# Kernel tuning notes

Hardware: AMD Instinct MI355X
Metric: run time of the kernel (lower is better)

## Reference

```python
import jax, jax.numpy as jnp
import numpy as np

B, SQ, C = 8, 4096, 1280
CAD = 2048
H, D = 20, 64          # heads x head_dim = hidden_size
NT = 4                 # num IP tokens
TXT = 77               # text tokens
IP_SCALE = 1.0


def setup_inputs() -> dict:
    key = jax.random.key(0)
    ks = jax.random.split(key, 9)
    s = 0.02
    return {
        "hidden_states": jax.random.normal(ks[0], (B, SQ, C), jnp.float32),
        "encoder_hidden_states": jax.random.normal(ks[1], (B, TXT + NT, CAD), jnp.float32),
        "Wq": jax.random.normal(ks[2], (C, C), jnp.float32) * s,
        "Wk": jax.random.normal(ks[3], (CAD, C), jnp.float32) * s,
        "Wv": jax.random.normal(ks[4], (CAD, C), jnp.float32) * s,
        "Wk_ip": jax.random.normal(ks[5], (CAD, C), jnp.float32) * s,
        "Wv_ip": jax.random.normal(ks[6], (CAD, C), jnp.float32) * s,
        "Wo": jax.random.normal(ks[7], (C, C), jnp.float32) * s,
        "bo": jnp.zeros((C,), jnp.float32),
    }


def _heads(x):
    # [b, s, C] -> [b, H, s, D]
    b, s, _ = x.shape
    return x.reshape(b, s, H, D).transpose(0, 2, 1, 3)


def _attend(q, k, v):
    scale = jnp.asarray(1.0 / np.sqrt(D), q.dtype)
    probs = jax.nn.softmax(jnp.einsum('bhqd,bhkd->bhqk', q, k) * scale, axis=-1)
    return jnp.einsum('bhqk,bhkd->bhqd', probs, v)


def reference(hidden_states, encoder_hidden_states, Wq, Wk, Wv, Wk_ip, Wv_ip, Wo, bo):
    residual = hidden_states
    txt = encoder_hidden_states[:, :-NT, :]   # [B, 77, CAD]
    ip = encoder_hidden_states[:, -NT:, :]    # [B, 4, CAD]

    q = _heads(hidden_states @ Wq)            # [B, H, SQ, D]
    k = _heads(txt @ Wk)
    v = _heads(txt @ Wv)
    out = _attend(q, k, v)                    # text branch

    ip_k = _heads(ip @ Wk_ip)
    ip_v = _heads(ip @ Wv_ip)
    out = out + IP_SCALE * _attend(q, ip_k, ip_v)  # IP-adapter branch

    b = out.shape[0]
    out = out.transpose(0, 2, 1, 3).reshape(b, SQ, C)  # merge heads
    out = out @ Wo + bo
    return out + residual
```

## Files before the change

kernel.cpp:

```cpp
#include <hip/hip_runtime.h>
#include <hip/hip_bf16.h>
#include <cstdint>
#include <cstddef>


typedef __bf16 bf16_t;
typedef __bf16 bf16x8 __attribute__((ext_vector_type(8)));
typedef __bf16 bf16x4 __attribute__((ext_vector_type(4)));
typedef float  f32x4  __attribute__((ext_vector_type(4)));
typedef unsigned int u32x4 __attribute__((ext_vector_type(4)));

using as3_void  = __attribute__((address_space(3))) void;
using as1_cvoid = const __attribute__((address_space(1))) void;

#define TXT_ 77

__device__ __forceinline__ bf16x8 ld16(const void* p) {
  u32x4 v = *(const u32x4*)p;
  return __builtin_bit_cast(bf16x8, v);
}

template <int EPI>
__global__ __launch_bounds__(512, 2)
void gemm256(const bf16_t* __restrict__ A, const bf16_t* __restrict__ Bt,
             void* __restrict__ Cout, int ntn, int N, int K,
             const float* __restrict__ bias, const void* __restrict__ residual)
{
  __shared__ __align__(16) char smem[131072];
  const int tid = threadIdx.x, lane = tid & 63, wid = tid >> 6;
  const int wm = wid >> 2, wn = wid & 3;

  const int nwg = gridDim.x;
  int g = blockIdx.x;
  if ((nwg & 7) == 0) g = (blockIdx.x & 7) * (nwg >> 3) + (blockIdx.x >> 3);
  const long bm = (long)(g / ntn) * 256;
  const long bn = (long)(g % ntn) * 256;
  const int NTk = K >> 5;

  const int srow = lane >> 2;
  const int scol = ((lane & 3) ^ ((lane >> 3) & 3)) * 8;

  auto stageA = [&](int t) {
    const int buf = t & 3;
    const long k0 = (long)t << 5;
#pragma unroll
    for (int j = 0; j < 2; ++j) {
      const int ci = j * 8 + wid;
      const bf16_t* gp = A + (bm + ci * 16 + srow) * (long)K + k0 + scol;
      __builtin_amdgcn_global_load_lds((as1_cvoid*)gp,
          (as3_void*)(smem + buf * 16384 + ci * 1024), 16, 0, 0);
    }
  };
  auto stageB = [&](int t) {
    const int buf = t & 3;
    const long k0 = (long)t << 5;
#pragma unroll
    for (int j = 0; j < 2; ++j) {
      const int ci = j * 8 + wid;
      const bf16_t* gp = Bt + (bn + ci * 16 + srow) * (long)K + k0 + scol;
      __builtin_amdgcn_global_load_lds((as1_cvoid*)gp,
          (as3_void*)(smem + 65536 + buf * 16384 + ci * 1024), 16, 0, 0);
    }
  };

  const int l15 = lane & 15, kq = lane >> 4;
  const int rc16 = (kq ^ ((l15 >> 1) & 3)) << 4;

  f32x4 acc[8][4] = {};
  bf16x8 afr[4], bfr[4];

  stageA(0); stageB(0); stageA(1); stageB(1);
  asm volatile("s_waitcnt vmcnt(4)" ::: "memory");
  __builtin_amdgcn_s_barrier();

  for (int t = 0; t < NTk; ++t) {
    const char* sa = smem + (t & 3) * 16384;
    const char* sb = smem + 65536 + (t & 3) * 16384;
    const bool pf = (t + 2 < NTk);

#pragma unroll
    for (int n = 0; n < 4; ++n)
      bfr[n] = ld16(sb + (wn * 64 + n * 16 + l15) * 64 + rc16);
#pragma unroll
    for (int m = 0; m < 4; ++m)
      afr[m] = ld16(sa + (wm * 128 + m * 16 + l15) * 64 + rc16);
    if (pf) stageA(t + 2);
    __builtin_amdgcn_s_setprio(1);
#pragma unroll
    for (int m = 0; m < 4; ++m)
#pragma unroll
      for (int n = 0; n < 4; ++n)
        acc[m][n] = __builtin_amdgcn_mfma_f32_16x16x32_bf16(afr[m], bfr[n], acc[m][n], 0, 0, 0);
    __builtin_amdgcn_s_setprio(0);

#pragma unroll
    for (int m = 0; m < 4; ++m)
      afr[m] = ld16(sa + (wm * 128 + (m + 4) * 16 + l15) * 64 + rc16);
    if (pf) stageB(t + 2);
    __builtin_amdgcn_s_setprio(1);
#pragma unroll
    for (int m = 0; m < 4; ++m)
#pragma unroll
      for (int n = 0; n < 4; ++n)
        acc[m + 4][n] = __builtin_amdgcn_mfma_f32_16x16x32_bf16(afr[m], bfr[n], acc[m + 4][n], 0, 0, 0);
    __builtin_amdgcn_s_setprio(0);

    if (t == NTk - 2) asm volatile("s_waitcnt vmcnt(0)" ::: "memory");
    else              asm volatile("s_waitcnt vmcnt(4)" ::: "memory");
    __builtin_amdgcn_s_barrier();
  }

  const int orow0 = (lane >> 4) << 2;
  if constexpr (EPI == 0) {
    bf16_t* cl = (bf16_t*)smem;
    const int lrow0 = wm * 128 + orow0;
    const int lcol0 = wn * 64 + l15;
#pragma unroll
    for (int m = 0; m < 8; ++m)
#pragma unroll
      for (int n = 0; n < 4; ++n)
#pragma unroll
        for (int r = 0; r < 4; ++r)
          cl[(lrow0 + m * 16 + r) * 256 + lcol0 + n * 16] = (bf16_t)acc[m][n][r];
    __syncthreads();
    const int rr = tid >> 5, cc = tid & 31;
#pragma unroll
    for (int s = 0; s < 16; ++s) {
      const int row = s * 16 + rr;
      const u32x4 v = *(const u32x4*)(cl + row * 256 + cc * 8);
      *(u32x4*)((bf16_t*)Cout + (bm + row) * (long)N + bn + cc * 8) = v;
    }
  } else {
#pragma unroll
    for (int m = 0; m < 8; ++m) {
#pragma unroll
      for (int n = 0; n < 4; ++n) {
        const long col = bn + wn * 64 + n * 16 + l15;
#pragma unroll
        for (int r = 0; r < 4; ++r) {
          const long row = bm + wm * 128 + m * 16 + orow0 + r;
          ((float*)Cout)[row * N + col] =
              acc[m][n][r] + bias[col] +
              (float)((const bf16_t*)residual)[row * N + col];
        }
      }
    }
  }
}

__global__ __launch_bounds__(256, 4)
void gemm_small(const bf16_t* __restrict__ A0, const bf16_t* __restrict__ B0,
                bf16_t* __restrict__ C0,
                const bf16_t* __restrict__ A1, const bf16_t* __restrict__ B1,
                bf16_t* __restrict__ C1)
{
  __shared__ __align__(16) char smem[2][16384];
  const int tid  = threadIdx.x;
  const int lane = tid & 63;
  const int wid  = tid >> 6;
  const int wm = wid >> 1, wn = wid & 1;

  const bf16_t *A, *Bt;
  bf16_t* Cout;
  int g = blockIdx.x;
  if (g < 100) { A = A0; Bt = B0; Cout = C0; }
  else         { A = A1; Bt = B1; Cout = C1; g -= 100; }
  const int ntn = 20, N = 2560, K = 2048;

  const long bm = (long)(g / ntn) * 128;
  const long bn = (long)(g % ntn) * 128;

  f32x4 acc[4][4] = {};

  const int srow = lane >> 2;
  const int skb  = (lane & 3) ^ (((lane >> 2) ^ (lane >> 4)) & 3);
  const int NT = K >> 5;

  auto stage = [&](int buf, int kt) {
    const int k0 = kt << 5;
#pragma unroll
    for (int cc = 0; cc < 2; ++cc) {
      const int c = wid + cc * 4;
      const bf16_t* ga = A + (bm + c * 16 + srow) * (long)K + (k0 + skb * 8);
      __builtin_amdgcn_global_load_lds((as1_cvoid*)ga,
                                       (as3_void*)(&smem[buf][c * 1024]), 16, 0, 0);
      const bf16_t* gb = Bt + (bn + c * 16 + srow) * (long)K + (k0 + skb * 8);
      __builtin_amdgcn_global_load_lds((as1_cvoid*)gb,
                                       (as3_void*)(&smem[buf][8192 + c * 1024]), 16, 0, 0);
    }
  };

  const int rkb    = (((lane >> 4) ^ (lane & 3) ^ ((lane >> 2) & 3)) & 3) << 4;
  const int rrow_a = wm * 64 + (lane & 15);
  const int rrow_b = wn * 64 + (lane & 15);

  stage(0, 0);
  int cur = 0;
  for (int t = 0; t < NT; ++t) {
    __syncthreads();
    if (t + 1 < NT) stage(cur ^ 1, t + 1);
    const char* sa = smem[cur];
    const char* sb = smem[cur] + 8192;
    bf16x8 af[4], bfv[4];
#pragma unroll
    for (int m = 0; m < 4; ++m)
      af[m] = ld16(sa + (rrow_a + m * 16) * 64 + rkb);
#pragma unroll
    for (int n = 0; n < 4; ++n)
      bfv[n] = ld16(sb + (rrow_b + n * 16) * 64 + rkb);
#pragma unroll
    for (int m = 0; m < 4; ++m)
#pragma unroll
      for (int n = 0; n < 4; ++n)
        acc[m][n] = __builtin_amdgcn_mfma_f32_16x16x32_bf16(af[m], bfv[n], acc[m][n], 0, 0, 0);
    cur ^= 1;
  }

  const int orow0 = wm * 64 + ((lane >> 4) << 2);
  const int ocol0 = wn * 64 + (lane & 15);
#pragma unroll
  for (int m = 0; m < 4; ++m)
#pragma unroll
    for (int n = 0; n < 4; ++n) {
      const long col = bn + ocol0 + n * 16;
#pragma unroll
      for (int r = 0; r < 4; ++r)
        Cout[(bm + orow0 + m * 16 + r) * (long)N + col] = (bf16_t)acc[m][n][r];
    }
}

__global__ __launch_bounds__(256, 3)
void attn_fused(const bf16_t* __restrict__ q, const bf16_t* __restrict__ kvt,
                const bf16_t* __restrict__ kvip, bf16_t* __restrict__ outp)
{
  __shared__ __align__(16) bf16_t K_lds[80 * 64];
  __shared__ __align__(16) bf16_t Kip_lds[16 * 64];
  __shared__ __align__(16) bf16_t Vt_lds[64 * 128];
  __shared__ __align__(16) bf16_t P_lds[4][16 * 128];

  const int tid = threadIdx.x, lane = tid & 63, wid = tid >> 6;
  const int h = blockIdx.y, b = blockIdx.z;
  const int kvcol = h << 6;

  for (int idx = tid; idx < 640; idx += 256) {
    const int j = idx >> 3, c = idx & 7;
    bf16x8 v = {};
    if (j < TXT_) v = ld16(kvt + (long)(b * 80 + j) * 2560 + kvcol + c * 8);
    *(bf16x8*)((char*)K_lds + j * 128 + ((c ^ (j & 7)) << 4)) = v;
  }
  if (tid < 128) {
    const int j = tid >> 3, c = tid & 7;
    bf16x8 v = {};
    if (j < 4) v = ld16(kvip + (long)(b * 4 + j) * 2560 + kvcol + c * 8);
    *(bf16x8*)((char*)Kip_lds + j * 128 + ((c ^ (j & 7)) << 4)) = v;
  }
  for (int idx = tid; idx < 1024; idx += 256) {
    const int key = idx >> 3, c = idx & 7;
    bf16x8 v = {};
    if (key < TXT_)
      v = ld16(kvt + (long)(b * 80 + key) * 2560 + 1280 + kvcol + c * 8);
    else if (key >= 96 && key < 100)
      v = ld16(kvip + (long)(b * 4 + key - 96) * 2560 + 1280 + kvcol + c * 8);
#pragma unroll
    for (int e = 0; e < 8; ++e) {
      const int d = c * 8 + e;
      *(bf16_t*)((char*)Vt_lds + d * 256 + ((key * 2) ^ ((d & 7) << 4))) = v[e];
    }
  }
  for (int idx = tid; idx < 1024; idx += 256)
    *(bf16x8*)((char*)P_lds + idx * 16) = (bf16x8){};
  __syncthreads();

  const int l15 = lane & 15, hi = lane >> 4;
  const int dblk = hi << 3;
  const int prow0 = hi << 2;
  const float scale = 0.125f;
  char* const pw = (char*)P_lds[wid];

  const long qrow0 = (long)b * 4096 + ((long)blockIdx.x << 8) + (wid << 6);
  bf16x8 qf[4][2];
#pragma unroll
  for (int ms = 0; ms < 4; ++ms) {
    const bf16_t* qp = q + (qrow0 + ms * 16 + l15) * 1280 + kvcol;
    qf[ms][0] = ld16(qp + dblk);
    qf[ms][1] = ld16(qp + 32 + dblk);
  }

#pragma unroll
  for (int ms = 0; ms < 4; ++ms) {
    f32x4 sc[5];
#pragma unroll
    for (int t = 0; t < 5; ++t) {
      const int j = (t << 4) + l15;
      const bf16x8 k0 = ld16((char*)K_lds + j * 128 + ((hi ^ (j & 7)) << 4));
      const bf16x8 k1 = ld16((char*)K_lds + j * 128 + (((4 + hi) ^ (j & 7)) << 4));
      f32x4 z = {0.f, 0.f, 0.f, 0.f};
      z = __builtin_amdgcn_mfma_f32_16x16x32_bf16(qf[ms][0], k0, z, 0, 0, 0);
      z = __builtin_amdgcn_mfma_f32_16x16x32_bf16(qf[ms][1], k1, z, 0, 0, 0);
      sc[t] = z;
    }
#pragma unroll
    for (int t = 0; t < 5; ++t) {
      const bool valid = ((t << 4) + l15) < TXT_;
#pragma unroll
      for (int r = 0; r < 4; ++r)
        sc[t][r] = valid ? sc[t][r] * scale : -1e30f;
    }

#pragma unroll
    for (int r = 0; r < 4; ++r) {
      float m = sc[0][r];
#pragma unroll
      for (int t = 1; t < 5; ++t) m = fmaxf(m, sc[t][r]);
      m = fmaxf(m, __shfl_xor(m, 1));
      m = fmaxf(m, __shfl_xor(m, 2));
      m = fmaxf(m, __shfl_xor(m, 4));
      m = fmaxf(m, __shfl_xor(m, 8));
      float l = 0.f;
#pragma unroll
      for (int t = 0; t < 5; ++t) { const float p = __expf(sc[t][r] - m); sc[t][r] = p; l += p; }
      l += __shfl_xor(l, 1);
      l += __shfl_xor(l, 2);
      l += __shfl_xor(l, 4);
      l += __shfl_xor(l, 8);
      const float inv = 1.f / l;
      const int row = prow0 + r;
#pragma unroll
      for (int t = 0; t < 5; ++t)
        *(bf16_t*)(pw + row * 256 + ((((t << 4) + l15) * 2) ^ ((row & 7) << 4))) =
            (bf16_t)(sc[t][r] * inv);
    }

    {
      const bf16x8 ki0 = ld16((char*)Kip_lds + l15 * 128 + ((hi ^ (l15 & 7)) << 4));
      const bf16x8 ki1 = ld16((char*)Kip_lds + l15 * 128 + (((4 + hi) ^ (l15 & 7)) << 4));
      f32x4 z = {0.f, 0.f, 0.f, 0.f};
      z = __builtin_amdgcn_mfma_f32_16x16x32_bf16(qf[ms][0], ki0, z, 0, 0, 0);
      z = __builtin_amdgcn_mfma_f32_16x16x32_bf16(qf[ms][1], ki1, z, 0, 0, 0);
      const bool vip = l15 < 4;
#pragma unroll
      for (int r = 0; r < 4; ++r) {
        const float s = vip ? z[r] * scale : -1e30f;
        float m = s;
        m = fmaxf(m, __shfl_xor(m, 1));
        m = fmaxf(m, __shfl_xor(m, 2));
        m = fmaxf(m, __shfl_xor(m, 4));
        m = fmaxf(m, __shfl_xor(m, 8));
        const float p = __expf(s - m);
        float l = p;
        l += __shfl_xor(l, 1);
        l += __shfl_xor(l, 2);
        l += __shfl_xor(l, 4);
        l += __shfl_xor(l, 8);
        const int row = prow0 + r;
        *(bf16_t*)(pw + row * 256 + (((96 + l15) * 2) ^ ((row & 7) << 4))) =
            (bf16_t)(p * (1.f / l));
      }
    }

    f32x4 o[4] = {};
#pragma unroll
    for (int s = 0; s < 4; ++s) {
      const bf16x8 pa =
          ld16(pw + l15 * 256 + ((((s << 2) + hi) << 4) ^ ((l15 & 7) << 4)));
#pragma unroll
      for (int n = 0; n < 4; ++n) {
        const int d = (n << 4) + l15;
        const bf16x8 vb =
            ld16((char*)Vt_lds + d * 256 + ((((s << 2) + hi) << 4) ^ ((d & 7) << 4)));
        o[n] = __builtin_amdgcn_mfma_f32_16x16x32_bf16(pa, vb, o[n], 0, 0, 0);
      }
    }

    const long orow = qrow0 + ms * 16 + prow0;
#pragma unroll
    for (int n = 0; n < 4; ++n)
#pragma unroll
      for (int r = 0; r < 4; ++r)
        outp[(orow + r) * 1280 + kvcol + (n << 4) + l15] = (bf16_t)o[n][r];
  }
}

__global__ void cvt_bf16(const float* __restrict__ in, bf16_t* __restrict__ out, long n)
{
  const long i = ((long)blockIdx.x * 256 + threadIdx.x) * 4;
  if (i >= n) return;
  const float4 v = *(const float4*)(in + i);
  bf16x4 r;
  r[0] = (bf16_t)v.x; r[1] = (bf16_t)v.y; r[2] = (bf16_t)v.z; r[3] = (bf16_t)v.w;
  *(bf16x4*)(out + i) = r;
}

__global__ void transpose_all(const float* __restrict__ Wq, const float* __restrict__ Wo,
                              const float* __restrict__ Wk, const float* __restrict__ Wv,
                              const float* __restrict__ Wki, const float* __restrict__ Wvi,
                              bf16_t* __restrict__ Wq_t, bf16_t* __restrict__ Wo_t,
                              bf16_t* __restrict__ Wkv_t, bf16_t* __restrict__ Wip_t)
{
  const int z = blockIdx.z;
  const float* in;
  bf16_t* out;
  int K;
  switch (z) {
    case 0:  in = Wq;  out = Wq_t;                        K = 1280; break;
    case 1:  in = Wo;  out = Wo_t;                        K = 1280; break;
    case 2:  in = Wk;  out = Wkv_t;                       K = 2048; break;
    case 3:  in = Wv;  out = Wkv_t + (long)1280 * 2048;   K = 2048; break;
    case 4:  in = Wki; out = Wip_t;                       K = 2048; break;
    default: in = Wvi; out = Wip_t + (long)1280 * 2048;   K = 2048; break;
  }
  const int k0 = blockIdx.x * 32, n0 = blockIdx.y * 32;
  if (k0 >= K) return;
  __shared__ float tile[32][33];
  for (int i = threadIdx.y; i < 32; i += 8)
    tile[i][threadIdx.x] = in[(long)(k0 + i) * 1280 + n0 + threadIdx.x];
  __syncthreads();
  for (int i = threadIdx.y; i < 32; i += 8)
    out[(long)(n0 + i) * K + k0 + threadIdx.x] = (bf16_t)tile[threadIdx.x][i];
}

__global__ void pack_enc(const float* __restrict__ enc, bf16_t* __restrict__ a_txt,
                         bf16_t* __restrict__ a_ip)
{
  const long t4 = ((long)blockIdx.x * 256 + threadIdx.x) * 4;
  const long NTXT = 640L * 2048;
  bf16x4 r;
  r[0] = r[1] = r[2] = r[3] = (bf16_t)0.f;
  if (t4 < NTXT) {
    const int row = (int)(t4 >> 11), col = (int)(t4 & 2047);
    const int b = row / 80, j = row - b * 80;
    if (j < TXT_) {
      const float4 v = *(const float4*)(enc + (((long)(b * 81 + j)) << 11) + col);
      r[0] = (bf16_t)v.x; r[1] = (bf16_t)v.y; r[2] = (bf16_t)v.z; r[3] = (bf16_t)v.w;
    }
    *(bf16x4*)(a_txt + t4) = r;
  } else {
    const long u = t4 - NTXT;
    const int row = (int)(u >> 11), col = (int)(u & 2047);
    if (row < 32) {
      const int b = row >> 2, j = row & 3;
      const float4 v = *(const float4*)(enc + (((long)(b * 81 + TXT_ + j)) << 11) + col);
      r[0] = (bf16_t)v.x; r[1] = (bf16_t)v.y; r[2] = (bf16_t)v.z; r[3] = (bf16_t)v.w;
    }
    *(bf16x4*)(a_ip + u) = r;
  }
}

extern "C" void kernel_launch(void* const* d_in, const int* in_sizes, int n_in,
                              void* d_out, int out_size, void* d_ws, size_t ws_size,
                              hipStream_t stream)
{
  (void)in_sizes; (void)n_in; (void)out_size; (void)ws_size;
  const float* hs  = (const float*)d_in[0];
  const float* enc = (const float*)d_in[1];
  const float* Wq  = (const float*)d_in[2];
  const float* Wk  = (const float*)d_in[3];
  const float* Wv  = (const float*)d_in[4];
  const float* Wki = (const float*)d_in[5];
  const float* Wvi = (const float*)d_in[6];
  const float* Wo  = (const float*)d_in[7];
  const float* bo  = (const float*)d_in[8];

  char* ws = (char*)d_ws;
  size_t off = 0;
  auto alloc = [&](size_t bytes) {
    char* p = ws + off;
    off += (bytes + 255) & ~(size_t)255;
    return p;
  };
  bf16_t* buf1   = (bf16_t*)alloc(83886080);
  bf16_t* qb     = (bf16_t*)alloc(83886080);
  bf16_t* Wq_t   = (bf16_t*)alloc(3276800);
  bf16_t* Wo_t   = (bf16_t*)alloc(3276800);
  bf16_t* Wkv_t  = (bf16_t*)alloc(10485760);
  bf16_t* Wip_t  = (bf16_t*)alloc(10485760);
  bf16_t* a_txt  = (bf16_t*)alloc(2621440);
  bf16_t* a_ip   = (bf16_t*)alloc(524288);
  bf16_t* kv_txt = (bf16_t*)alloc(3276800);
  bf16_t* kv_ip  = (bf16_t*)alloc(655360);

  cvt_bf16<<<40960, 256, 0, stream>>>(hs, buf1, 41943040L);
  transpose_all<<<dim3(64, 40, 6), dim3(32, 8), 0, stream>>>(
      Wq, Wo, Wk, Wv, Wki, Wvi, Wq_t, Wo_t, Wkv_t, Wip_t);
  pack_enc<<<1536, 256, 0, stream>>>(enc, a_txt, a_ip);

  gemm256<0><<<640, 512, 0, stream>>>(buf1, Wq_t, qb, 5, 1280, 1280,
                                      nullptr, nullptr);
  gemm_small<<<120, 256, 0, stream>>>(a_txt, Wkv_t, kv_txt, a_ip, Wip_t, kv_ip);

  attn_fused<<<dim3(16, 20, 8), 256, 0, stream>>>(qb, kv_txt, kv_ip, qb);

  gemm256<2><<<640, 512, 0, stream>>>(qb, Wo_t, d_out, 5, 1280, 1280,
                                      bo, buf1);
}
```

Measured before the change: 439.8 us.

## Fuse fp32-to-bf16 conversion of hidden states into Q-projection GEMM A-loading

Removes the standalone cvt_bf16 pass over hidden_states. The Q GEMM now loads fp32 A tiles into registers, converts them to bf16 and writes them to LDS itself, and the output GEMM reads the fp32 residual directly. This cuts a full read/write pass over the 168MB input and its bf16 copy. In exchange, the Q GEMM A path moves from direct global-to-LDS loads to register staging, with twice the global bytes per tile and extra VGPR pressure.

Result: slower. 470.7 us (+7.0%).

```diff
diff --git a/kernel.cpp b/kernel.cpp
--- a/kernel.cpp
+++ b/kernel.cpp
@@ -20,11 +20,11 @@
   return __builtin_bit_cast(bf16x8, v);
 }
 
-template <int EPI>
+template <int EPI, int AF32>
 __global__ __launch_bounds__(512, 2)
-void gemm256(const bf16_t* __restrict__ A, const bf16_t* __restrict__ Bt,
+void gemm256(const void* __restrict__ Ap, const bf16_t* __restrict__ Bt,
              void* __restrict__ Cout, int ntn, int N, int K,
-             const float* __restrict__ bias, const void* __restrict__ residual)
+             const float* __restrict__ bias, const float* __restrict__ residual)
 {
   __shared__ __align__(16) char smem[131072];
   const int tid = threadIdx.x, lane = tid & 63, wid = tid >> 6;
@@ -40,13 +40,13 @@
   const int srow = lane >> 2;
   const int scol = ((lane & 3) ^ ((lane >> 3) & 3)) * 8;
 
-  auto stageA = [&](int t) {
+  auto stageA16 = [&](int t) {
     const int buf = t & 3;
     const long k0 = (long)t << 5;
 #pragma unroll
     for (int j = 0; j < 2; ++j) {
       const int ci = j * 8 + wid;
-      const bf16_t* gp = A + (bm + ci * 16 + srow) * (long)K + k0 + scol;
+      const bf16_t* gp = (const bf16_t*)Ap + (bm + ci * 16 + srow) * (long)K + k0 + scol;
       __builtin_amdgcn_global_load_lds((as1_cvoid*)gp,
           (as3_void*)(smem + buf * 16384 + ci * 1024), 16, 0, 0);
     }
@@ -63,14 +63,47 @@
     }
   };
 
+  f32x4 aP[2][2];
+  auto issueA = [&](int t) {
+#pragma unroll
+    for (int j = 0; j < 2; ++j) {
+      const int ci = j * 8 + wid;
+      const float* gp = (const float*)Ap + (bm + ci * 16 + srow) * (long)K + ((long)t << 5) + scol;
+      aP[j][0] = *(const f32x4*)gp;
+      aP[j][1] = *(const f32x4*)(gp + 4);
+    }
+  };
+  auto writeA = [&](int t) {
+    const int buf = t & 3;
+#pragma unroll
+    for (int j = 0; j < 2; ++j) {
+      const int ci = j * 8 + wid;
+      bf16x8 v;
+      v[0] = (bf16_t)aP[j][0][0]; v[1] = (bf16_t)aP[j][0][1];
+      v[2] = (bf16_t)aP[j][0][2]; v[3] = (bf16_t)aP[j][0][3];
+      v[4] = (bf16_t)aP[j][1][0]; v[5] = (bf16_t)aP[j][1][1];
+      v[6] = (bf16_t)aP[j][1][2]; v[7] = (bf16_t)aP[j][1][3];
+      *(bf16x8*)(smem + buf * 16384 + ci * 1024 + lane * 16) = v;
+    }
+  };
+
   const int l15 = lane & 15, kq = lane >> 4;
   const int rc16 = (kq ^ ((l15 >> 1) & 3)) << 4;
 
   f32x4 acc[8][4] = {};
   bf16x8 afr[4], bfr[4];
 
-  stageA(0); stageB(0); stageA(1); stageB(1);
-  asm volatile("s_waitcnt vmcnt(4)" ::: "memory");
+  if constexpr (AF32) {
+    issueA(0);
+    writeA(0);
+    issueA(1);
+    stageB(0); stageB(1);
+    asm volatile("s_waitcnt vmcnt(2)" ::: "memory");
+    asm volatile("s_waitcnt lgkmcnt(0)" ::: "memory");
+  } else {
+    stageA16(0); stageB(0); stageA16(1); stageB(1);
+    asm volatile("s_waitcnt vmcnt(4)" ::: "memory");
+  }
   __builtin_amdgcn_s_barrier();
 
   for (int t = 0; t < NTk; ++t) {
@@ -84,7 +117,12 @@
 #pragma unroll
     for (int m = 0; m < 4; ++m)
       afr[m] = ld16(sa + (wm * 128 + m * 16 + l15) * 64 + rc16);
-    if (pf) stageA(t + 2);
+    if constexpr (AF32) {
+      if (t + 1 < NTk) writeA(t + 1);
+      if (pf) { issueA(t + 2); stageB(t + 2); }
+    } else {
+      if (pf) stageA16(t + 2);
+    }
     __builtin_amdgcn_s_setprio(1);
 #pragma unroll
     for (int m = 0; m < 4; ++m)
@@ -96,7 +134,9 @@
 #pragma unroll
     for (int m = 0; m < 4; ++m)
       afr[m] = ld16(sa + (wm * 128 + (m + 4) * 16 + l15) * 64 + rc16);
-    if (pf) stageB(t + 2);
+    if constexpr (!AF32) {
+      if (pf) stageB(t + 2);
+    }
     __builtin_amdgcn_s_setprio(1);
 #pragma unroll
     for (int m = 0; m < 4; ++m)
@@ -105,8 +145,15 @@
         acc[m + 4][n] = __builtin_amdgcn_mfma_f32_16x16x32_bf16(afr[m], bfr[n], acc[m + 4][n], 0, 0, 0);
     __builtin_amdgcn_s_setprio(0);
 
-    if (t == NTk - 2) asm volatile("s_waitcnt vmcnt(0)" ::: "memory");
-    else              asm volatile("s_waitcnt vmcnt(4)" ::: "memory");
+    __builtin_amdgcn_sched_barrier(0);
+    if constexpr (AF32) {
+      if (pf) asm volatile("s_waitcnt vmcnt(6)" ::: "memory");
+      else    asm volatile("s_waitcnt vmcnt(0)" ::: "memory");
+      asm volatile("s_waitcnt lgkmcnt(0)" ::: "memory");
+    } else {
+      if (t == NTk - 2) asm volatile("s_waitcnt vmcnt(0)" ::: "memory");
+      else              asm volatile("s_waitcnt vmcnt(4)" ::: "memory");
+    }
     __builtin_amdgcn_s_barrier();
   }
 
@@ -140,8 +187,7 @@
         for (int r = 0; r < 4; ++r) {
           const long row = bm + wm * 128 + m * 16 + orow0 + r;
           ((float*)Cout)[row * N + col] =
-              acc[m][n][r] + bias[col] +
-              (float)((const bf16_t*)residual)[row * N + col];
+              acc[m][n][r] + bias[col] + residual[row * N + col];
         }
       }
     }
@@ -381,16 +427,6 @@
   }
 }
 
-__global__ void cvt_bf16(const float* __restrict__ in, bf16_t* __restrict__ out, long n)
-{
-  const long i = ((long)blockIdx.x * 256 + threadIdx.x) * 4;
-  if (i >= n) return;
-  const float4 v = *(const float4*)(in + i);
-  bf16x4 r;
-  r[0] = (bf16_t)v.x; r[1] = (bf16_t)v.y; r[2] = (bf16_t)v.z; r[3] = (bf16_t)v.w;
-  *(bf16x4*)(out + i) = r;
-}
-
 __global__ void transpose_all(const float* __restrict__ Wq, const float* __restrict__ Wo,
                               const float* __restrict__ Wk, const float* __restrict__ Wv,
                               const float* __restrict__ Wki, const float* __restrict__ Wvi,
@@ -468,7 +504,6 @@
     off += (bytes + 255) & ~(size_t)255;
     return p;
   };
-  bf16_t* buf1   = (bf16_t*)alloc(83886080);
   bf16_t* qb     = (bf16_t*)alloc(83886080);
   bf16_t* Wq_t   = (bf16_t*)alloc(3276800);
   bf16_t* Wo_t   = (bf16_t*)alloc(3276800);
@@ -479,17 +514,16 @@
   bf16_t* kv_txt = (bf16_t*)alloc(3276800);
   bf16_t* kv_ip  = (bf16_t*)alloc(655360);
 
-  cvt_bf16<<<40960, 256, 0, stream>>>(hs, buf1, 41943040L);
   transpose_all<<<dim3(64, 40, 6), dim3(32, 8), 0, stream>>>(
       Wq, Wo, Wk, Wv, Wki, Wvi, Wq_t, Wo_t, Wkv_t, Wip_t);
   pack_enc<<<1536, 256, 0, stream>>>(enc, a_txt, a_ip);
 
-  gemm256<0><<<640, 512, 0, stream>>>(buf1, Wq_t, qb, 5, 1280, 1280,
-                                      nullptr, nullptr);
+  gemm256<0, 1><<<640, 512, 0, stream>>>(hs, Wq_t, qb, 5, 1280, 1280,
+                                         nullptr, nullptr);
   gemm_small<<<120, 256, 0, stream>>>(a_txt, Wkv_t, kv_txt, a_ip, Wip_t, kv_ip);
 
   attn_fused<<<dim3(16, 20, 8), 256, 0, stream>>>(qb, kv_txt, kv_ip, qb);
 
-  gemm256<2><<<640, 512, 0, stream>>>(qb, Wo_t, d_out, 5, 1280, 1280,
-                                      bo, buf1);
-}
+  gemm256<2, 0><<<640, 512, 0, stream>>>(qb, Wo_t, d_out, 5, 1280, 1280,
+                                         bo, hs);
+}
```

## Merge prep kernels into one launch and fold KV projections into Q GEMM

Applied to the files above, without the earlier changes.

Combines the bf16 conversion, weight transposes and encoder packing into a single prep kernel. It also runs the text and IP K/V projections as extra 256x256 tiles of the Q-projection GEMM launch, so one grid of 680 blocks replaces two launches. The KV buffers are padded to 256-row multiples to fit the larger tile. This cuts launch count and lets the small KV GEMM overlap the tail of the large one. The cost is wasted compute on the padded KV tiles and a heavier per-block setup.

Result: faster. 421.9 us, median of 2 (-4.1%).

```diff
diff --git a/kernel.cpp b/kernel.cpp
--- a/kernel.cpp
+++ b/kernel.cpp
@@ -21,18 +21,14 @@
 }
 
 template <int EPI>
-__global__ __launch_bounds__(512, 2)
-void gemm256(const bf16_t* __restrict__ A, const bf16_t* __restrict__ Bt,
-             void* __restrict__ Cout, int ntn, int N, int K,
-             const float* __restrict__ bias, const void* __restrict__ residual)
-{
-  __shared__ __align__(16) char smem[131072];
+__device__ __forceinline__ void gemm256_body(
+    char* smem, const bf16_t* __restrict__ A, const bf16_t* __restrict__ Bt,
+    void* __restrict__ Cout, int g, int ntn, int N, int K,
+    const float* __restrict__ bias, const bf16_t* __restrict__ residual)
+{
   const int tid = threadIdx.x, lane = tid & 63, wid = tid >> 6;
   const int wm = wid >> 2, wn = wid & 3;
 
-  const int nwg = gridDim.x;
-  int g = blockIdx.x;
-  if ((nwg & 7) == 0) g = (blockIdx.x & 7) * (nwg >> 3) + (blockIdx.x >> 3);
   const long bm = (long)(g / ntn) * 256;
   const long bn = (long)(g % ntn) * 256;
   const int NTk = K >> 5;
@@ -140,93 +136,46 @@
         for (int r = 0; r < 4; ++r) {
           const long row = bm + wm * 128 + m * 16 + orow0 + r;
           ((float*)Cout)[row * N + col] =
-              acc[m][n][r] + bias[col] +
-              (float)((const bf16_t*)residual)[row * N + col];
+              acc[m][n][r] + bias[col] + (float)residual[row * N + col];
         }
       }
     }
   }
 }
 
-__global__ __launch_bounds__(256, 4)
-void gemm_small(const bf16_t* __restrict__ A0, const bf16_t* __restrict__ B0,
-                bf16_t* __restrict__ C0,
-                const bf16_t* __restrict__ A1, const bf16_t* __restrict__ B1,
-                bf16_t* __restrict__ C1)
-{
-  __shared__ __align__(16) char smem[2][16384];
-  const int tid  = threadIdx.x;
-  const int lane = tid & 63;
-  const int wid  = tid >> 6;
-  const int wm = wid >> 1, wn = wid & 1;
-
+__global__ __launch_bounds__(512, 2)
+void gemm1_fused(const bf16_t* __restrict__ hsb, const bf16_t* __restrict__ Wq_t,
+                 bf16_t* __restrict__ qb,
+                 const bf16_t* __restrict__ a_txt, const bf16_t* __restrict__ Wkv_t,
+                 bf16_t* __restrict__ kv_txt,
+                 const bf16_t* __restrict__ a_ip, const bf16_t* __restrict__ Wip_t,
+                 bf16_t* __restrict__ kv_ip)
+{
+  __shared__ __align__(16) char smem[131072];
+  const int bid = blockIdx.x;
   const bf16_t *A, *Bt;
-  bf16_t* Cout;
-  int g = blockIdx.x;
-  if (g < 100) { A = A0; Bt = B0; Cout = C0; }
-  else         { A = A1; Bt = B1; Cout = C1; g -= 100; }
-  const int ntn = 20, N = 2560, K = 2048;
-
-  const long bm = (long)(g / ntn) * 128;
-  const long bn = (long)(g % ntn) * 128;
-
-  f32x4 acc[4][4] = {};
-
-  const int srow = lane >> 2;
-  const int skb  = (lane & 3) ^ (((lane >> 2) ^ (lane >> 4)) & 3);
-  const int NT = K >> 5;
-
-  auto stage = [&](int buf, int kt) {
-    const int k0 = kt << 5;
-#pragma unroll
-    for (int cc = 0; cc < 2; ++cc) {
-      const int c = wid + cc * 4;
-      const bf16_t* ga = A + (bm + c * 16 + srow) * (long)K + (k0 + skb * 8);
-      __builtin_amdgcn_global_load_lds((as1_cvoid*)ga,
-                                       (as3_void*)(&smem[buf][c * 1024]), 16, 0, 0);
-      const bf16_t* gb = Bt + (bn + c * 16 + srow) * (long)K + (k0 + skb * 8);
-      __builtin_amdgcn_global_load_lds((as1_cvoid*)gb,
-                                       (as3_void*)(&smem[buf][8192 + c * 1024]), 16, 0, 0);
-    }
-  };
-
-  const int rkb    = (((lane >> 4) ^ (lane & 3) ^ ((lane >> 2) & 3)) & 3) << 4;
-  const int rrow_a = wm * 64 + (lane & 15);
-  const int rrow_b = wn * 64 + (lane & 15);
-
-  stage(0, 0);
-  int cur = 0;
-  for (int t = 0; t < NT; ++t) {
-    __syncthreads();
-    if (t + 1 < NT) stage(cur ^ 1, t + 1);
-    const char* sa = smem[cur];
-    const char* sb = smem[cur] + 8192;
-    bf16x8 af[4], bfv[4];
-#pragma unroll
-    for (int m = 0; m < 4; ++m)
-      af[m] = ld16(sa + (rrow_a + m * 16) * 64 + rkb);
-#pragma unroll
-    for (int n = 0; n < 4; ++n)
-      bfv[n] = ld16(sb + (rrow_b + n * 16) * 64 + rkb);
-#pragma unroll
-    for (int m = 0; m < 4; ++m)
-#pragma unroll
-      for (int n = 0; n < 4; ++n)
-        acc[m][n] = __builtin_amdgcn_mfma_f32_16x16x32_bf16(af[m], bfv[n], acc[m][n], 0, 0, 0);
-    cur ^= 1;
-  }
-
-  const int orow0 = wm * 64 + ((lane >> 4) << 2);
-  const int ocol0 = wn * 64 + (lane & 15);
-#pragma unroll
-  for (int m = 0; m < 4; ++m)
-#pragma unroll
-    for (int n = 0; n < 4; ++n) {
-      const long col = bn + ocol0 + n * 16;
-#pragma unroll
-      for (int r = 0; r < 4; ++r)
-        Cout[(bm + orow0 + m * 16 + r) * (long)N + col] = (bf16_t)acc[m][n][r];
-    }
+  bf16_t* C;
+  int g, ntn, N, K;
+  if (bid < 640) {
+    g = (bid & 7) * 80 + (bid >> 3);
+    A = hsb; Bt = Wq_t; C = qb; ntn = 5; N = 1280; K = 1280;
+  } else if (bid < 670) {
+    g = bid - 640; A = a_txt; Bt = Wkv_t; C = kv_txt; ntn = 10; N = 2560; K = 2048;
+  } else {
+    g = bid - 670; A = a_ip; Bt = Wip_t; C = kv_ip; ntn = 10; N = 2560; K = 2048;
+  }
+  gemm256_body<0>(smem, A, Bt, C, g, ntn, N, K, nullptr, nullptr);
+}
+
+__global__ __launch_bounds__(512, 2)
+void gemm2(const bf16_t* __restrict__ A, const bf16_t* __restrict__ Bt,
+           float* __restrict__ Cout, const float* __restrict__ bias,
+           const bf16_t* __restrict__ residual)
+{
+  __shared__ __align__(16) char smem[131072];
+  const int bid = blockIdx.x;
+  const int g = (bid & 7) * 80 + (bid >> 3);
+  gemm256_body<2>(smem, A, Bt, Cout, g, 5, 1280, 1280, bias, residual);
 }
 
 __global__ __launch_bounds__(256, 3)
@@ -381,68 +330,74 @@
   }
 }
 
-__global__ void cvt_bf16(const float* __restrict__ in, bf16_t* __restrict__ out, long n)
-{
-  const long i = ((long)blockIdx.x * 256 + threadIdx.x) * 4;
-  if (i >= n) return;
-  const float4 v = *(const float4*)(in + i);
-  bf16x4 r;
-  r[0] = (bf16_t)v.x; r[1] = (bf16_t)v.y; r[2] = (bf16_t)v.z; r[3] = (bf16_t)v.w;
-  *(bf16x4*)(out + i) = r;
-}
-
-__global__ void transpose_all(const float* __restrict__ Wq, const float* __restrict__ Wo,
-                              const float* __restrict__ Wk, const float* __restrict__ Wv,
-                              const float* __restrict__ Wki, const float* __restrict__ Wvi,
-                              bf16_t* __restrict__ Wq_t, bf16_t* __restrict__ Wo_t,
-                              bf16_t* __restrict__ Wkv_t, bf16_t* __restrict__ Wip_t)
-{
-  const int z = blockIdx.z;
-  const float* in;
-  bf16_t* out;
-  int K;
-  switch (z) {
-    case 0:  in = Wq;  out = Wq_t;                        K = 1280; break;
-    case 1:  in = Wo;  out = Wo_t;                        K = 1280; break;
-    case 2:  in = Wk;  out = Wkv_t;                       K = 2048; break;
-    case 3:  in = Wv;  out = Wkv_t + (long)1280 * 2048;   K = 2048; break;
-    case 4:  in = Wki; out = Wip_t;                       K = 2048; break;
-    default: in = Wvi; out = Wip_t + (long)1280 * 2048;   K = 2048; break;
-  }
-  const int k0 = blockIdx.x * 32, n0 = blockIdx.y * 32;
-  if (k0 >= K) return;
+__global__ __launch_bounds__(256)
+void prep(const float* __restrict__ hs, bf16_t* __restrict__ hsb,
+          const float* __restrict__ Wq, const float* __restrict__ Wo,
+          const float* __restrict__ Wk, const float* __restrict__ Wv,
+          const float* __restrict__ Wki, const float* __restrict__ Wvi,
+          bf16_t* __restrict__ Wq_t, bf16_t* __restrict__ Wo_t,
+          bf16_t* __restrict__ Wkv_t, bf16_t* __restrict__ Wip_t,
+          const float* __restrict__ enc, bf16_t* __restrict__ a_txt,
+          bf16_t* __restrict__ a_ip)
+{
   __shared__ float tile[32][33];
-  for (int i = threadIdx.y; i < 32; i += 8)
-    tile[i][threadIdx.x] = in[(long)(k0 + i) * 1280 + n0 + threadIdx.x];
-  __syncthreads();
-  for (int i = threadIdx.y; i < 32; i += 8)
-    out[(long)(n0 + i) * K + k0 + threadIdx.x] = (bf16_t)tile[threadIdx.x][i];
-}
-
-__global__ void pack_enc(const float* __restrict__ enc, bf16_t* __restrict__ a_txt,
-                         bf16_t* __restrict__ a_ip)
-{
-  const long t4 = ((long)blockIdx.x * 256 + threadIdx.x) * 4;
-  const long NTXT = 640L * 2048;
-  bf16x4 r;
-  r[0] = r[1] = r[2] = r[3] = (bf16_t)0.f;
-  if (t4 < NTXT) {
-    const int row = (int)(t4 >> 11), col = (int)(t4 & 2047);
-    const int b = row / 80, j = row - b * 80;
-    if (j < TXT_) {
-      const float4 v = *(const float4*)(enc + (((long)(b * 81 + j)) << 11) + col);
-      r[0] = (bf16_t)v.x; r[1] = (bf16_t)v.y; r[2] = (bf16_t)v.z; r[3] = (bf16_t)v.w;
-    }
-    *(bf16x4*)(a_txt + t4) = r;
+  const int bid = blockIdx.x, tid = threadIdx.x;
+
+  if (bid < 40960) {
+    const long i = ((long)bid * 256 + tid) * 4;
+    const float4 v = *(const float4*)(hs + i);
+    bf16x4 r;
+    r[0] = (bf16_t)v.x; r[1] = (bf16_t)v.y; r[2] = (bf16_t)v.z; r[3] = (bf16_t)v.w;
+    *(bf16x4*)(hsb + i) = r;
+  } else if (bid < 56320) {
+    const int idx = bid - 40960;
+    const int z = idx / 2560, rem = idx % 2560;
+    const int kx = rem & 63, ny = rem >> 6;
+    const float* in;
+    bf16_t* out;
+    int K;
+    switch (z) {
+      case 0:  in = Wq;  out = Wq_t;                      K = 1280; break;
+      case 1:  in = Wo;  out = Wo_t;                      K = 1280; break;
+      case 2:  in = Wk;  out = Wkv_t;                     K = 2048; break;
+      case 3:  in = Wv;  out = Wkv_t + (long)1280 * 2048; K = 2048; break;
+      case 4:  in = Wki; out = Wip_t;                     K = 2048; break;
+      default: in = Wvi; out = Wip_t + (long)1280 * 2048; K = 2048; break;
+    }
+    const int k0 = kx * 32, n0 = ny * 32;
+    if (k0 < K) {
+      const int tx = tid & 31, ty = tid >> 5;
+      for (int i = ty; i < 32; i += 8)
+        tile[i][tx] = in[(long)(k0 + i) * 1280 + n0 + tx];
+      __syncthreads();
+      for (int i = ty; i < 32; i += 8)
+        out[(long)(n0 + i) * K + k0 + tx] = (bf16_t)tile[tx][i];
+    }
   } else {
-    const long u = t4 - NTXT;
-    const int row = (int)(u >> 11), col = (int)(u & 2047);
-    if (row < 32) {
-      const int b = row >> 2, j = row & 3;
-      const float4 v = *(const float4*)(enc + (((long)(b * 81 + TXT_ + j)) << 11) + col);
-      r[0] = (bf16_t)v.x; r[1] = (bf16_t)v.y; r[2] = (bf16_t)v.z; r[3] = (bf16_t)v.w;
-    }
-    *(bf16x4*)(a_ip + u) = r;
+    const long t4 = ((long)(bid - 56320) * 256 + tid) * 4;
+    const long NTXT = 768L * 2048;
+    bf16x4 r;
+    r[0] = r[1] = r[2] = r[3] = (bf16_t)0.f;
+    if (t4 < NTXT) {
+      const int row = (int)(t4 >> 11), col = (int)(t4 & 2047);
+      if (row < 640) {
+        const int b = row / 80, j = row - b * 80;
+        if (j < TXT_) {
+          const float4 v = *(const float4*)(enc + (((long)(b * 81 + j)) << 11) + col);
+          r[0] = (bf16_t)v.x; r[1] = (bf16_t)v.y; r[2] = (bf16_t)v.z; r[3] = (bf16_t)v.w;
+        }
+      }
+      *(bf16x4*)(a_txt + t4) = r;
+    } else {
+      const long u = t4 - NTXT;
+      const int row = (int)(u >> 11), col = (int)(u & 2047);
+      if (row < 32) {
+        const int b = row >> 2, j = row & 3;
+        const float4 v = *(const float4*)(enc + (((long)(b * 81 + TXT_ + j)) << 11) + col);
+        r[0] = (bf16_t)v.x; r[1] = (bf16_t)v.y; r[2] = (bf16_t)v.z; r[3] = (bf16_t)v.w;
+      }
+      *(bf16x4*)(a_ip + u) = r;
+    }
   }
 }
 
@@ -474,22 +429,19 @@
   bf16_t* Wo_t   = (bf16_t*)alloc(3276800);
   bf16_t* Wkv_t  = (bf16_t*)alloc(10485760);
   bf16_t* Wip_t  = (bf16_t*)alloc(10485760);
-  bf16_t* a_txt  = (bf16_t*)alloc(2621440);
-  bf16_t* a_ip   = (bf16_t*)alloc(524288);
-  bf16_t* kv_txt = (bf16_t*)alloc(3276800);
-  bf16_t* kv_ip  = (bf16_t*)alloc(655360);
-
-  cvt_bf16<<<40960, 256, 0, stream>>>(hs, buf1, 41943040L);
-  transpose_all<<<dim3(64, 40, 6), dim3(32, 8), 0, stream>>>(
-      Wq, Wo, Wk, Wv, Wki, Wvi, Wq_t, Wo_t, Wkv_t, Wip_t);
-  pack_enc<<<1536, 256, 0, stream>>>(enc, a_txt, a_ip);
-
-  gemm256<0><<<640, 512, 0, stream>>>(buf1, Wq_t, qb, 5, 1280, 1280,
-                                      nullptr, nullptr);
-  gemm_small<<<120, 256, 0, stream>>>(a_txt, Wkv_t, kv_txt, a_ip, Wip_t, kv_ip);
+  bf16_t* a_txt  = (bf16_t*)alloc(3145728);
+  bf16_t* a_ip   = (bf16_t*)alloc(1048576);
+  bf16_t* kv_txt = (bf16_t*)alloc(3932160);
+  bf16_t* kv_ip  = (bf16_t*)alloc(1310720);
+
+  prep<<<58368, 256, 0, stream>>>(hs, buf1, Wq, Wo, Wk, Wv, Wki, Wvi,
+                                  Wq_t, Wo_t, Wkv_t, Wip_t, enc, a_txt, a_ip);
+
+  gemm1_fused<<<680, 512, 0, stream>>>(buf1, Wq_t, qb,
+                                       a_txt, Wkv_t, kv_txt,
+                                       a_ip, Wip_t, kv_ip);
 
   attn_fused<<<dim3(16, 20, 8), 256, 0, stream>>>(qb, kv_txt, kv_ip, qb);
 
-  gemm256<2><<<640, 512, 0, stream>>>(qb, Wo_t, d_out, 5, 1280, 1280,
-                                      bo, buf1);
-}
+  gemm2<<<640, 512, 0, stream>>>(qb, Wo_t, (float*)d_out, bo, buf1);
+}
```
